# Performance work log

Hardware: AMD Instinct MI355X
Metric: run time of the kernel (lower is better)

## Reference

```python
import jax, jax.numpy as jnp
import numpy as np

D = 1024  # input_dim

def setup_inputs() -> dict:
    key = jax.random.key(0)
    ks = jax.random.split(key, 8)
    x = jax.random.normal(ks[0], (8, 2048, D), dtype=jnp.float32)
    q = jax.random.normal(ks[1], (8, 1024, D), dtype=jnp.float32)
    s = 1.0 / np.sqrt(D)
    Wq = jax.random.normal(ks[2], (D, D), dtype=jnp.float32) * s
    bq = jnp.zeros((D,), dtype=jnp.float32)
    Wk = jax.random.normal(ks[3], (D, D), dtype=jnp.float32) * s
    bk = jnp.zeros((D,), dtype=jnp.float32)
    Wv = jax.random.normal(ks[4], (D, D), dtype=jnp.float32) * s
    bv = jnp.zeros((D,), dtype=jnp.float32)
    return {"x": x, "q": q, "Wq": Wq, "bq": bq, "Wk": Wk, "bk": bk, "Wv": Wv, "bv": bv}

def reference(x, q, Wq, bq, Wk, bk, Wv, bv):
    # Linear layers: y = in @ W^T + b (torch nn.Linear convention)
    queries = jnp.einsum('bqd,ed->bqe', q, Wq) + bq   # [B, Lq, D]
    keys    = jnp.einsum('bkd,ed->bke', x, Wk) + bk   # [B, Lk, D]
    values  = jnp.einsum('bkd,ed->bke', x, Wv) + bv   # [B, Lk, D]
    scale = 1.0 / jnp.sqrt(jnp.asarray(D, dtype=queries.dtype))
    scores = jnp.einsum('bqd,bkd->bqk', queries, keys) * scale  # [B, Lq, Lk]
    attention = jax.nn.softmax(scores, axis=2)
    weighted = jnp.einsum('bqk,bkd->bqd', attention, values)    # [B, Lq, D]
    return (weighted, jnp.squeeze(attention, axis=1) if attention.shape[1] == 1 else attention)
```

## Files before the change

kernel.cpp:

```cpp
#include <hip/hip_runtime.h>
#include <hip/hip_bf16.h>

typedef __attribute__((ext_vector_type(8))) short short8;
typedef __attribute__((ext_vector_type(4))) short short4v;
typedef __attribute__((ext_vector_type(4))) float f32x4;
using u16 = unsigned short;

__device__ __forceinline__ u16 f2bf(float x) {
    __hip_bfloat16 h = __float2bfloat16(x);
    return *reinterpret_cast<u16*>(&h);
}

__device__ __forceinline__ void async16(void* lds, const void* g) {
    __builtin_amdgcn_global_load_lds((__attribute__((address_space(1))) void*)g,
                                     (__attribute__((address_space(3))) void*)lds,
                                     16, 0, 0);
}

__global__ __launch_bounds__(256)
void f32_to_bf16_kernel(const float* __restrict__ in, u16* __restrict__ out, long n) {
    long i = ((long)blockIdx.x * 256 + threadIdx.x) * 8;
    if (i + 8 > n) return;
    float4 a = *(const float4*)(in + i);
    float4 b = *(const float4*)(in + i + 4);
    short8 p;
    p[0] = (short)f2bf(a.x); p[1] = (short)f2bf(a.y);
    p[2] = (short)f2bf(a.z); p[3] = (short)f2bf(a.w);
    p[4] = (short)f2bf(b.x); p[5] = (short)f2bf(b.y);
    p[6] = (short)f2bf(b.z); p[7] = (short)f2bf(b.w);
    *(short8*)(out + i) = p;
}

template<bool A_F32, bool OUT_BF16, bool ADD_BIAS, bool KV_FUSED>
__global__ __launch_bounds__(256, 2)
void gemm_bt_kernel(const void* __restrict__ Av, const u16* __restrict__ B,
                    void* __restrict__ Cv, u16* __restrict__ C2,
                    const float* __restrict__ bias, const float* __restrict__ bias2,
                    float scale, int M, int N, int K,
                    long Abatch, long Bbatch, long Cbatch)
{
    __shared__ u16 As[128 * 32];
    __shared__ u16 Bs[128 * 32];

    int bx = blockIdx.x, by = blockIdx.y, bz = blockIdx.z;
    {
        const int gx = gridDim.x, gy = gridDim.y;
        const int nwg = gx * gy * gridDim.z;
        if ((nwg & 7) == 0) {
            const int b = bx + gx * (by + gy * bz);
            const int cpx = nwg >> 3;
            const int s = (b & 7) * cpx + (b >> 3);
            bx = s % gx;
            const int t = s / gx;
            by = t % gy;
            bz = t / gy;
        }
    }

    const int tid  = threadIdx.x;
    const int wid  = tid >> 6;
    const int lane = tid & 63;

    B += (long)bz * Bbatch;

    const int bm = by * 128;
    const int bn = bx * 128;

    const int wr = (wid >> 1) * 64;
    const int wc = (wid & 1) * 64;

    f32x4 acc[4][4] = {};

    const int srow = tid >> 2;
    const int scol = (tid & 3) * 8;
    const u16*   aptrb = nullptr;
    const float* aptrf = nullptr;
    if constexpr (A_F32) {
        aptrf = (const float*)Av + (long)bz * Abatch + (long)(bm + srow) * K + scol;
    } else {
        aptrb = (const u16*)Av + (long)bz * Abatch + (long)(bm + srow) * K + scol;
    }
    const u16* bptr = B + (long)(bn + srow) * K + scol;
    char* asb = (char*)As + wid * 1024;
    char* bsb = (char*)Bs + wid * 1024;

    const int lr = lane & 15;
    const int lk = (lane >> 4) * 8;

    const int nk = K >> 5;
    for (int kt = 0; kt < nk; ++kt) {
        const u16* bk = bptr + kt * 32;
        async16(bsb,        bk);
        async16(bsb + 4096, bk + (long)64 * K);
        if constexpr (A_F32) {
            const float* a0 = aptrf + kt * 32;
            float4 u0 = *(const float4*)a0;
            float4 u1 = *(const float4*)(a0 + 4);
            float4 w0 = *(const float4*)(a0 + (long)64 * K);
            float4 w1 = *(const float4*)(a0 + (long)64 * K + 4);
            short8 s0, s1;
            s0[0] = (short)f2bf(u0.x); s0[1] = (short)f2bf(u0.y);
            s0[2] = (short)f2bf(u0.z); s0[3] = (short)f2bf(u0.w);
            s0[4] = (short)f2bf(u1.x); s0[5] = (short)f2bf(u1.y);
            s0[6] = (short)f2bf(u1.z); s0[7] = (short)f2bf(u1.w);
            s1[0] = (short)f2bf(w0.x); s1[1] = (short)f2bf(w0.y);
            s1[2] = (short)f2bf(w0.z); s1[3] = (short)f2bf(w0.w);
            s1[4] = (short)f2bf(w1.x); s1[5] = (short)f2bf(w1.y);
            s1[6] = (short)f2bf(w1.z); s1[7] = (short)f2bf(w1.w);
            *(short8*)((char*)As + tid * 16)        = s0;
            *(short8*)((char*)As + 4096 + tid * 16) = s1;
        } else {
            const u16* ak = aptrb + kt * 32;
            async16(asb,        ak);
            async16(asb + 4096, ak + (long)64 * K);
        }
        __syncthreads();

        short8 af[4], bfr[4];
        #pragma unroll
        for (int i = 0; i < 4; ++i)
            af[i] = *(const short8*)&As[(wr + i * 16 + lr) * 32 + lk];
        #pragma unroll
        for (int j = 0; j < 4; ++j)
            bfr[j] = *(const short8*)&Bs[(wc + j * 16 + lr) * 32 + lk];

        #pragma unroll
        for (int i = 0; i < 4; ++i)
            #pragma unroll
            for (int j = 0; j < 4; ++j)
                acc[i][j] = __builtin_amdgcn_mfma_f32_16x16x32_bf16(
                                af[i], bfr[j], acc[i][j], 0, 0, 0);
        __syncthreads();
    }

    const int r0 = (lane >> 4) * 4;
    const long crow = bm + wr + r0;
    const long ccol = bn + wc + lr;
    if constexpr (KV_FUSED) {
        if (bn < 1024) {
            u16* C = (u16*)Cv;
            #pragma unroll
            for (int i = 0; i < 4; ++i)
                #pragma unroll
                for (int j = 0; j < 4; ++j) {
                    const float bb = bias[ccol + j * 16];
                    #pragma unroll
                    for (int r = 0; r < 4; ++r)
                        C[(crow + i * 16 + r) * 1024L + ccol + j * 16] =
                            f2bf(acc[i][j][r] + bb);
                }
        } else {
            #pragma unroll
            for (int i = 0; i < 4; ++i) {
                const long row = crow + i * 16;
                const long zb = row >> 11, rr = row & 2047;
                #pragma unroll
                for (int j = 0; j < 4; ++j) {
                    const long feat = ccol - 1024 + j * 16;
                    const float bb = bias2[feat];
                    short4v pk;
                    #pragma unroll
                    for (int r = 0; r < 4; ++r)
                        pk[r] = (short)f2bf(acc[i][j][r] + bb);
                    *(short4v*)(C2 + zb * 2097152 + feat * 2048 + rr) = pk;
                }
            }
        }
    } else if constexpr (OUT_BF16) {
        u16* C = (u16*)Cv + (long)bz * Cbatch;
        #pragma unroll
        for (int i = 0; i < 4; ++i)
            #pragma unroll
            for (int j = 0; j < 4; ++j) {
                float bb = 0.f;
                if constexpr (ADD_BIAS) bb = bias[ccol + j * 16];
                #pragma unroll
                for (int r = 0; r < 4; ++r)
                    C[(crow + i * 16 + r) * (long)N + ccol + j * 16] =
                        f2bf(acc[i][j][r] * scale + bb);
            }
    } else {
        float* C = (float*)Cv + (long)bz * Cbatch;
        #pragma unroll
        for (int i = 0; i < 4; ++i)
            #pragma unroll
            for (int j = 0; j < 4; ++j) {
                float bb = 0.f;
                if constexpr (ADD_BIAS) bb = bias[ccol + j * 16];
                #pragma unroll
                for (int r = 0; r < 4; ++r)
                    C[(crow + i * 16 + r) * (long)N + ccol + j * 16] =
                        acc[i][j][r] * scale + bb;
            }
    }
}

__global__ __launch_bounds__(256)
void softmax_kernel(float* __restrict__ S, int L) {
    const long base = (long)blockIdx.x * L;
    float* row = S + base;
    const int t = threadIdx.x;
    const int lane = t & 63, wid = t >> 6;

    float4 v0 = ((const float4*)row)[2 * t];
    float4 v1 = ((const float4*)row)[2 * t + 1];

    float m = fmaxf(fmaxf(fmaxf(v0.x, v0.y), fmaxf(v0.z, v0.w)),
                    fmaxf(fmaxf(v1.x, v1.y), fmaxf(v1.z, v1.w)));
    #pragma unroll
    for (int off = 32; off; off >>= 1) m = fmaxf(m, __shfl_xor(m, off));

    __shared__ float red[8];
    if (lane == 0) red[wid] = m;
    __syncthreads();
    m = fmaxf(fmaxf(red[0], red[1]), fmaxf(red[2], red[3]));

    v0.x = __expf(v0.x - m); v0.y = __expf(v0.y - m);
    v0.z = __expf(v0.z - m); v0.w = __expf(v0.w - m);
    v1.x = __expf(v1.x - m); v1.y = __expf(v1.y - m);
    v1.z = __expf(v1.z - m); v1.w = __expf(v1.w - m);

    float s = ((v0.x + v0.y) + (v0.z + v0.w)) + ((v1.x + v1.y) + (v1.z + v1.w));
    #pragma unroll
    for (int off = 32; off; off >>= 1) s += __shfl_xor(s, off);
    if (lane == 0) red[4 + wid] = s;
    __syncthreads();
    s = (red[4] + red[5]) + (red[6] + red[7]);

    const float inv = 1.0f / s;
    v0.x *= inv; v0.y *= inv; v0.z *= inv; v0.w *= inv;
    v1.x *= inv; v1.y *= inv; v1.z *= inv; v1.w *= inv;

    ((float4*)row)[2 * t]     = v0;
    ((float4*)row)[2 * t + 1] = v1;
}

extern "C" void kernel_launch(void* const* d_in, const int* in_sizes, int n_in,
                              void* d_out, int out_size, void* d_ws, size_t ws_size,
                              hipStream_t stream) {
    const float* x  = (const float*)d_in[0];
    const float* q  = (const float*)d_in[1];
    const float* Wq = (const float*)d_in[2];
    const float* bq = (const float*)d_in[3];
    const float* Wk = (const float*)d_in[4];
    const float* bk = (const float*)d_in[5];
    const float* Wv = (const float*)d_in[6];
    const float* bv = (const float*)d_in[7];
    float* out = (float*)d_out;

    u16* ws  = (u16*)d_ws;
    u16* wqb = ws;
    u16* wkb = ws + 1048576;
    u16* wvb = ws + 2097152;
    u16* Qbf = ws + 3145728;
    u16* Kbf = ws + 11534336;
    u16* Vt  = ws + 28311552;

    float* Sout = out + 8388608;

    dim3 blk(256);

    f32_to_bf16_kernel<<<512, blk, 0, stream>>>(Wq, wqb, 1048576L);
    f32_to_bf16_kernel<<<512, blk, 0, stream>>>(Wk, wkb, 1048576L);
    f32_to_bf16_kernel<<<512, blk, 0, stream>>>(Wv, wvb, 1048576L);

    gemm_bt_kernel<true, true, true, false><<<dim3(8, 64, 1), blk, 0, stream>>>(
        q, wqb, Qbf, nullptr, bq, nullptr, 1.0f, 8192, 1024, 1024, 0, 0, 0);

    gemm_bt_kernel<true, true, true, true><<<dim3(16, 128, 1), blk, 0, stream>>>(
        x, wkb, Kbf, Vt, bk, bv, 1.0f, 16384, 2048, 1024, 0, 0, 0);

    gemm_bt_kernel<false, false, false, false><<<dim3(16, 8, 8), blk, 0, stream>>>(
        Qbf, Kbf, Sout, nullptr, nullptr, nullptr, 0.03125f, 1024, 2048, 1024,
        1048576, 2097152, 2097152);

    softmax_kernel<<<8192, blk, 0, stream>>>(Sout, 2048);

    gemm_bt_kernel<true, false, false, false><<<dim3(8, 8, 8), blk, 0, stream>>>(
        Sout, Vt, out, nullptr, nullptr, nullptr, 1.0f, 1024, 1024, 2048,
        2097152, 2097152, 1048576);
}
```

Before: 446.6 us.

## Pre-convert activations to bf16 and load all GEMM operands asynchronously to LDS

The fp32 A-operand path in the GEMM, which loaded fp32 into registers, converted to bf16 and stored to LDS, is removed. x and q are now converted to bf16 up front into scratch space inside the output buffer. The softmax kernel also writes a bf16 copy of the probabilities, so every GEMM uses direct global-to-LDS async loads for both operands. This adds extra conversion passes and memory traffic in exchange for a simpler, higher-throughput GEMM inner loop. The scheme depends on reusing output and workspace regions (Pbf overlays Qbf) in the correct order.

```diff
diff --git a/kernel.cpp b/kernel.cpp
--- a/kernel.cpp
+++ b/kernel.cpp
@@ -31,9 +31,9 @@
     *(short8*)(out + i) = p;
 }
 
-template<bool A_F32, bool OUT_BF16, bool ADD_BIAS, bool KV_FUSED>
+template<bool OUT_BF16, bool ADD_BIAS, bool KV_FUSED>
 __global__ __launch_bounds__(256, 2)
-void gemm_bt_kernel(const void* __restrict__ Av, const u16* __restrict__ B,
+void gemm_bt_kernel(const u16* __restrict__ A, const u16* __restrict__ B,
                     void* __restrict__ Cv, u16* __restrict__ C2,
                     const float* __restrict__ bias, const float* __restrict__ bias2,
                     float scale, int M, int N, int K,
@@ -61,6 +61,7 @@
     const int wid  = tid >> 6;
     const int lane = tid & 63;
 
+    A += (long)bz * Abatch;
     B += (long)bz * Bbatch;
 
     const int bm = by * 128;
@@ -73,13 +74,7 @@
 
     const int srow = tid >> 2;
     const int scol = (tid & 3) * 8;
-    const u16*   aptrb = nullptr;
-    const float* aptrf = nullptr;
-    if constexpr (A_F32) {
-        aptrf = (const float*)Av + (long)bz * Abatch + (long)(bm + srow) * K + scol;
-    } else {
-        aptrb = (const u16*)Av + (long)bz * Abatch + (long)(bm + srow) * K + scol;
-    }
+    const u16* aptr = A + (long)(bm + srow) * K + scol;
     const u16* bptr = B + (long)(bn + srow) * K + scol;
     char* asb = (char*)As + wid * 1024;
     char* bsb = (char*)Bs + wid * 1024;
@@ -89,31 +84,12 @@
 
     const int nk = K >> 5;
     for (int kt = 0; kt < nk; ++kt) {
+        const u16* ak = aptr + kt * 32;
         const u16* bk = bptr + kt * 32;
+        async16(asb,        ak);
+        async16(asb + 4096, ak + (long)64 * K);
         async16(bsb,        bk);
         async16(bsb + 4096, bk + (long)64 * K);
-        if constexpr (A_F32) {
-            const float* a0 = aptrf + kt * 32;
-            float4 u0 = *(const float4*)a0;
-            float4 u1 = *(const float4*)(a0 + 4);
-            float4 w0 = *(const float4*)(a0 + (long)64 * K);
-            float4 w1 = *(const float4*)(a0 + (long)64 * K + 4);
-            short8 s0, s1;
-            s0[0] = (short)f2bf(u0.x); s0[1] = (short)f2bf(u0.y);
-            s0[2] = (short)f2bf(u0.z); s0[3] = (short)f2bf(u0.w);
-            s0[4] = (short)f2bf(u1.x); s0[5] = (short)f2bf(u1.y);
-            s0[6] = (short)f2bf(u1.z); s0[7] = (short)f2bf(u1.w);
-            s1[0] = (short)f2bf(w0.x); s1[1] = (short)f2bf(w0.y);
-            s1[2] = (short)f2bf(w0.z); s1[3] = (short)f2bf(w0.w);
-            s1[4] = (short)f2bf(w1.x); s1[5] = (short)f2bf(w1.y);
-            s1[6] = (short)f2bf(w1.z); s1[7] = (short)f2bf(w1.w);
-            *(short8*)((char*)As + tid * 16)        = s0;
-            *(short8*)((char*)As + 4096 + tid * 16) = s1;
-        } else {
-            const u16* ak = aptrb + kt * 32;
-            async16(asb,        ak);
-            async16(asb + 4096, ak + (long)64 * K);
-        }
         __syncthreads();
 
         short8 af[4], bfr[4];
@@ -196,7 +172,7 @@
 }
 
 __global__ __launch_bounds__(256)
-void softmax_kernel(float* __restrict__ S, int L) {
+void softmax_kernel(float* __restrict__ S, u16* __restrict__ P, int L) {
     const long base = (long)blockIdx.x * L;
     float* row = S + base;
     const int t = threadIdx.x;
@@ -233,6 +209,13 @@
 
     ((float4*)row)[2 * t]     = v0;
     ((float4*)row)[2 * t + 1] = v1;
+
+    short8 p;
+    p[0] = (short)f2bf(v0.x); p[1] = (short)f2bf(v0.y);
+    p[2] = (short)f2bf(v0.z); p[3] = (short)f2bf(v0.w);
+    p[4] = (short)f2bf(v1.x); p[5] = (short)f2bf(v1.y);
+    p[6] = (short)f2bf(v1.z); p[7] = (short)f2bf(v1.w);
+    *(short8*)(P + base + 8 * t) = p;
 }
 
 extern "C" void kernel_launch(void* const* d_in, const int* in_sizes, int n_in,
@@ -254,29 +237,34 @@
     u16* wvb = ws + 2097152;
     u16* Qbf = ws + 3145728;
     u16* Kbf = ws + 11534336;
+    u16* Pbf = ws + 3145728;
     u16* Vt  = ws + 28311552;
 
     float* Sout = out + 8388608;
+    u16*   xbf  = (u16*)Sout;
+    u16*   qbf  = (u16*)out;
 
     dim3 blk(256);
 
-    f32_to_bf16_kernel<<<512, blk, 0, stream>>>(Wq, wqb, 1048576L);
-    f32_to_bf16_kernel<<<512, blk, 0, stream>>>(Wk, wkb, 1048576L);
-    f32_to_bf16_kernel<<<512, blk, 0, stream>>>(Wv, wvb, 1048576L);
-
-    gemm_bt_kernel<true, true, true, false><<<dim3(8, 64, 1), blk, 0, stream>>>(
-        q, wqb, Qbf, nullptr, bq, nullptr, 1.0f, 8192, 1024, 1024, 0, 0, 0);
-
-    gemm_bt_kernel<true, true, true, true><<<dim3(16, 128, 1), blk, 0, stream>>>(
-        x, wkb, Kbf, Vt, bk, bv, 1.0f, 16384, 2048, 1024, 0, 0, 0);
-
-    gemm_bt_kernel<false, false, false, false><<<dim3(16, 8, 8), blk, 0, stream>>>(
+    f32_to_bf16_kernel<<<8192, blk, 0, stream>>>(x,  xbf, 16777216L);
+    f32_to_bf16_kernel<<<4096, blk, 0, stream>>>(q,  qbf,  8388608L);
+    f32_to_bf16_kernel<<<512,  blk, 0, stream>>>(Wq, wqb,  1048576L);
+    f32_to_bf16_kernel<<<512,  blk, 0, stream>>>(Wk, wkb,  1048576L);
+    f32_to_bf16_kernel<<<512,  blk, 0, stream>>>(Wv, wvb,  1048576L);
+
+    gemm_bt_kernel<true, true, false><<<dim3(8, 64, 1), blk, 0, stream>>>(
+        qbf, wqb, Qbf, nullptr, bq, nullptr, 1.0f, 8192, 1024, 1024, 0, 0, 0);
+
+    gemm_bt_kernel<true, true, true><<<dim3(16, 128, 1), blk, 0, stream>>>(
+        xbf, wkb, Kbf, Vt, bk, bv, 1.0f, 16384, 2048, 1024, 0, 0, 0);
+
+    gemm_bt_kernel<false, false, false><<<dim3(16, 8, 8), blk, 0, stream>>>(
         Qbf, Kbf, Sout, nullptr, nullptr, nullptr, 0.03125f, 1024, 2048, 1024,
         1048576, 2097152, 2097152);
 
-    softmax_kernel<<<8192, blk, 0, stream>>>(Sout, 2048);
-
-    gemm_bt_kernel<true, false, false, false><<<dim3(8, 8, 8), blk, 0, stream>>>(
-        Sout, Vt, out, nullptr, nullptr, nullptr, 1.0f, 1024, 1024, 2048,
+    softmax_kernel<<<8192, blk, 0, stream>>>(Sout, Pbf, 2048);
+
+    gemm_bt_kernel<false, false, false><<<dim3(8, 8, 8), blk, 0, stream>>>(
+        Pbf, Vt, out, nullptr, nullptr, nullptr, 1.0f, 1024, 1024, 2048,
         2097152, 2097152, 1048576);
 }
```

Result: faster. 413.2 us (-7.5%).
